# Kernel optimization log

Measured on AMD Instinct MI355X. Metric: run time of the kernel, lower is better.

The kernel has to match this reference:

```python
import jax, jax.numpy as jnp
import numpy as np

B, S, H = 32, 2048, 1024

def setup_inputs() -> dict:
    key = jax.random.key(0)
    k1, k2, k3, k4, k5 = jax.random.split(key, 5)
    return {
        "hidden": jax.random.normal(k1, (B, H), dtype=jnp.float32),
        "encoder_outputs": jax.random.normal(k2, (B, S, H), dtype=jnp.float32),
        "W_attn": jax.random.normal(k3, (H, H), dtype=jnp.float32) * (1.0 / np.sqrt(H)),
        "b_attn": jax.random.normal(k4, (H,), dtype=jnp.float32) * 0.01,
        "v": jax.random.uniform(k5, (H,), dtype=jnp.float32),
    }

def reference(hidden, encoder_outputs, W_attn, b_attn, v):
    # energy = tanh((enc + hidden[:,None,:]) @ W^T + b)  -> [B,S,H]
    x = encoder_outputs + hidden[:, None, :]
    energy = jnp.tanh(jnp.einsum('bsh,oh->bso', x, W_attn) + b_attn)
    scores = jnp.einsum('bsh,h->bs', energy, v)            # [B,S]
    attn_weights = jax.nn.softmax(scores, axis=1)          # [B,S]
    context = jnp.einsum('bs,bsh->bh', attn_weights, encoder_outputs)  # [B,H]
    return (context, attn_weights)
```

## Files before the change

### kernel.cpp

```cpp
#include <hip/hip_runtime.h>
#include <hip/hip_bf16.h>

#define BATCH 32
#define SEQ   2048
#define HID   1024
#define M_TOT (BATCH*SEQ)
#define NG    32

typedef __attribute__((ext_vector_type(8))) short          bf16x8;
typedef __attribute__((ext_vector_type(8))) unsigned short us8;
typedef __attribute__((ext_vector_type(4))) float          f32x4;

__device__ __forceinline__ unsigned short f2bf_rn(float x) {
    unsigned u = __float_as_uint(x);
    return (unsigned short)((u + 0x7fffu + ((u >> 16) & 1u)) >> 16);
}
__device__ __forceinline__ float bf2f(unsigned short h) {
    return __uint_as_float(((unsigned)h) << 16);
}
__device__ __forceinline__ unsigned cvt_pk_bf16(float s0, float s1) {
    unsigned r;
    asm("v_cvt_pk_bf16_f32 %0, %1, %2" : "=v"(r) : "v"(s0), "v"(s1));
    return r;
}

using as1_cv = const __attribute__((address_space(1))) void;
using as3_v  = __attribute__((address_space(3))) void;
__device__ __forceinline__ void gload16(const void* g, char* s) {
    __builtin_amdgcn_global_load_lds((as1_cv*)g, (as3_v*)s, 16, 0, 0);
}

#define FENCE() asm volatile("" ::: "memory")
#define BAR_P()  do { FENCE(); __builtin_amdgcn_s_barrier(); FENCE(); } while (0)
#define BAR_LG() do { asm volatile("s_waitcnt lgkmcnt(0)" ::: "memory"); \
                      __builtin_amdgcn_s_barrier(); FENCE(); } while (0)
#define BAR_VM8() do { asm volatile("s_waitcnt vmcnt(8) lgkmcnt(0)" ::: "memory"); \
                       __builtin_amdgcn_s_barrier(); FENCE(); } while (0)

#define MFMA_BLK(A4, B4, IB) do { \
  _Pragma("unroll") for (int i_ = 0; i_ < 4; i_++) \
  _Pragma("unroll") for (int j_ = 0; j_ < 4; j_++) \
    acc[(IB) + i_][j_] = __builtin_amdgcn_mfma_f32_16x16x32_bf16(A4[i_], B4[j_], acc[(IB)+i_][j_], 0, 0, 0); \
} while (0)

__global__ __launch_bounds__(256) void k_convW(const float* __restrict__ W,
                                               unsigned short* __restrict__ w2) {
    const int i8 = (blockIdx.x * 256 + threadIdx.x) * 8;
    const int o = i8 >> 10, h = i8 & 1023;
    float4 w0 = *(const float4*)(W + i8);
    float4 w1 = *(const float4*)(W + i8 + 4);
    float xs[8] = {w0.x, w0.y, w0.z, w0.w, w1.x, w1.y, w1.z, w1.w};
    us8 hv{}, lv{};
#pragma unroll
    for (int t = 0; t < 8; t++) {
        unsigned short xh = f2bf_rn(xs[t]);
        hv[t] = (unsigned short)xh;
        lv[t] = (unsigned short)f2bf_rn(xs[t] - bf2f(xh));
    }
    *(us8*)(w2 + (size_t)o * 2048 + h)        = hv;
    *(us8*)(w2 + (size_t)o * 2048 + 1024 + h) = lv;
}

__global__ __launch_bounds__(512, 2) void k_gemm_scores(
    const float* __restrict__ enc,
    const float* __restrict__ hidden,
    const unsigned short* __restrict__ w2,
    const float* __restrict__ b_attn,
    const float* __restrict__ v,
    float* __restrict__ pscore16)
{
    extern __shared__ char smem[];
    float* hidL = (float*)(smem + 131072);

    const int tid  = threadIdx.x;
    const int lane = tid & 63, wid = tid >> 6;
    const int wr = wid >> 2, wc = wid & 3;
    const int fr = lane & 15, g = lane >> 4;
    const int gxr = (fr >> 1) & 3;
    const int gsw = (g ^ gxr) * 16;

    const int bid  = blockIdx.x;
    const int swz  = (bid & 7) * 128 + (bid >> 3);
    const int mbase = (swz >> 2) * 256;
    const int nbase = (swz & 3) * 256;
    const int bidx  = mbase >> 11;

    const int arow = tid >> 1;
    const int acol = (tid & 1) * 16;
    const int axr  = (arow >> 1) & 3;
    const int ao0  = (((tid & 1) * 2) ^ axr) * 16;
    const int ao1  = ao0 ^ 16;
    const float* encP = enc + (size_t)(mbase + arow) * HID + acol;

    const int brow  = wid * 16 + (lane >> 2);
    const int bsx8  = ((lane & 3) ^ ((lane >> 3) & 3)) * 8;

    *(float2*)(hidL + tid * 2) = *(const float2*)(hidden + (size_t)bidx * HID + tid * 2);

    f32x4 acc[8][4];
#pragma unroll
    for (int i = 0; i < 8; i++)
#pragma unroll
        for (int j = 0; j < 4; j++) acc[i][j] = (f32x4)0.f;

    float4 er[4];

    auto loadEnc = [&](int Gn) {
        const float* ep = encP + Gn * 32;
#pragma unroll
        for (int q = 0; q < 4; q++) er[q] = *(const float4*)(ep + q * 4);
    };
    auto convA = [&](int Gn) {
        char* ap = smem + (Gn & 1) * 32768 + arow * 64;
        const float* hp = hidL + Gn * 32 + acol;
        unsigned hpk[8], lpk[8];
#pragma unroll
        for (int q = 0; q < 4; q++) {
            float4 e = er[q];
            float4 h = *(const float4*)(hp + q * 4);
            float x0 = e.x + h.x, x1 = e.y + h.y;
            float x2 = e.z + h.z, x3 = e.w + h.w;
            unsigned p01 = cvt_pk_bf16(x0, x1);
            unsigned p23 = cvt_pk_bf16(x2, x3);
            float h0 = __uint_as_float(p01 << 16);
            float h1 = __uint_as_float(p01 & 0xffff0000u);
            float h2 = __uint_as_float(p23 << 16);
            float h3 = __uint_as_float(p23 & 0xffff0000u);
            hpk[q * 2]     = p01;
            hpk[q * 2 + 1] = p23;
            lpk[q * 2]     = cvt_pk_bf16(x0 - h0, x1 - h1);
            lpk[q * 2 + 1] = cvt_pk_bf16(x2 - h2, x3 - h3);
        }
        *(uint4*)(ap + ao0)          = make_uint4(hpk[0], hpk[1], hpk[2], hpk[3]);
        *(uint4*)(ap + ao1)          = make_uint4(hpk[4], hpk[5], hpk[6], hpk[7]);
        *(uint4*)(ap + 16384 + ao0)  = make_uint4(lpk[0], lpk[1], lpk[2], lpk[3]);
        *(uint4*)(ap + 16384 + ao1)  = make_uint4(lpk[4], lpk[5], lpk[6], lpk[7]);
    };
    auto stageB = [&](int G2, int part) {
        const unsigned short* s0 = w2 + (size_t)(nbase + brow) * 2048 + part * 1024 + G2 * 32 + bsx8;
        char* d0 = smem + 65536 + (G2 & 1) * 32768 + part * 16384 + wid * 1024;
        gload16(s0, d0);
        gload16(s0 + (size_t)128 * 2048, d0 + 8192);
    };
    auto rdA = [&](int slot, int part, int i) -> bf16x8 {
        return *(const bf16x8*)(smem + slot * 32768 + part * 16384 +
                                (wr * 128 + i * 16 + fr) * 64 + gsw);
    };
    auto rdB = [&](int slot, int part, int j) -> bf16x8 {
        return *(const bf16x8*)(smem + 65536 + slot * 32768 + part * 16384 +
                                (wc * 64 + j * 16 + fr) * 64 + gsw);
    };

    loadEnc(0);
    stageB(0, 0); stageB(0, 1);
    stageB(1, 0); stageB(1, 1);
    asm volatile("s_waitcnt lgkmcnt(0)" ::: "memory");
    __builtin_amdgcn_s_barrier(); FENCE();
    convA(0);
    loadEnc(1);

    bf16x8 aa[4], aa2[4], bh[4], bl[4];

    for (int G = 0; G < NG; ++G) {
        const int slot = G & 1;
        const int Gs = (G + 2 < NG) ? G + 2 : G;
        const int Ge = (G + 2 < NG) ? G + 2 : NG - 1;
        BAR_VM8();
#pragma unroll
        for (int i = 0; i < 4; i++) aa[i] = rdA(slot, 0, i);
#pragma unroll
        for (int j = 0; j < 4; j++) bh[j] = rdB(slot, 0, j);
#pragma unroll
        for (int j = 0; j < 4; j++) bl[j] = rdB(slot, 1, j);
        __builtin_amdgcn_s_setprio(1);
        MFMA_BLK(aa, bh, 0);
        __builtin_amdgcn_s_setprio(0);
        BAR_LG();
        stageB(Gs, 0);
        __builtin_amdgcn_s_setprio(1);
        MFMA_BLK(aa, bl, 0);
        __builtin_amdgcn_s_setprio(0);
        BAR_P();
#pragma unroll
        for (int i = 0; i < 4; i++) aa2[i] = rdA(slot, 0, 4 + i);
        stageB(Gs, 1);
        __builtin_amdgcn_s_setprio(1);
        MFMA_BLK(aa2, bh, 4);
        __builtin_amdgcn_s_setprio(0);
        BAR_P();
        if (G + 1 < NG) convA(G + 1);
        loadEnc(Ge);
        __builtin_amdgcn_s_setprio(1);
        MFMA_BLK(aa2, bl, 4);
        __builtin_amdgcn_s_setprio(0);
        BAR_P();
#pragma unroll
        for (int i = 0; i < 4; i++) aa[i] = rdA(slot, 1, i);
        __builtin_amdgcn_s_setprio(1);
        MFMA_BLK(aa, bh, 0);
        __builtin_amdgcn_s_setprio(0);
#pragma unroll
        for (int i = 0; i < 4; i++) aa2[i] = rdA(slot, 1, 4 + i);
        __builtin_amdgcn_s_setprio(1);
        MFMA_BLK(aa2, bh, 4);
        __builtin_amdgcn_s_setprio(0);
    }

    float rs[8][4];
#pragma unroll
    for (int i = 0; i < 8; i++)
#pragma unroll
        for (int r = 0; r < 4; r++) rs[i][r] = 0.f;

#pragma unroll
    for (int j = 0; j < 4; j++) {
        const int n = nbase + wc * 64 + j * 16 + fr;
        const float ba = b_attn[n];
        const float vv = v[n];
#pragma unroll
        for (int i = 0; i < 8; i++)
#pragma unroll
            for (int r = 0; r < 4; r++) {
                float e  = acc[i][j][r] + ba;
                float ex = __expf(2.f * e);
                rs[i][r] += (1.f - 2.f / (ex + 1.f)) * vv;
            }
    }
#pragma unroll
    for (int off = 1; off < 16; off <<= 1)
#pragma unroll
        for (int i = 0; i < 8; i++)
#pragma unroll
            for (int r = 0; r < 4; r++) rs[i][r] += __shfl_xor(rs[i][r], off, 64);

    float v0 = 0.f, v1 = 0.f;
#pragma unroll
    for (int i = 0; i < 4; i++)
#pragma unroll
        for (int r = 0; r < 4; r++)
            if (fr == i * 4 + r) { v0 = rs[i][r]; v1 = rs[i + 4][r]; }

    const int plane = (swz & 3) * 4 + wc;
    const size_t pb = (size_t)plane * M_TOT + mbase + wr * 128 + g * 4 + (fr & 3);
    pscore16[pb + (fr >> 2) * 16]      = v0;
    pscore16[pb + (fr >> 2) * 16 + 64] = v1;
}

__global__ __launch_bounds__(256) void k_softmax(const float* __restrict__ ps,
                                                 float* __restrict__ out) {
    const int b = blockIdx.x, t = threadIdx.x;
    __shared__ float red[8];
    float loc[8];
    float lmax = -1e30f;
#pragma unroll
    for (int i = 0; i < 8; i++) {
        const int s = t + i * 256;
        float sc = 0.f;
#pragma unroll
        for (int p = 0; p < 16; p++) sc += ps[(size_t)p * M_TOT + (size_t)b * SEQ + s];
        loc[i] = sc;
        lmax = fmaxf(lmax, sc);
    }
    for (int o = 32; o; o >>= 1) lmax = fmaxf(lmax, __shfl_xor(lmax, o, 64));
    if ((t & 63) == 0) red[t >> 6] = lmax;
    __syncthreads();
    const float bmax = fmaxf(fmaxf(red[0], red[1]), fmaxf(red[2], red[3]));
    float ev[8], lsum = 0.f;
#pragma unroll
    for (int i = 0; i < 8; i++) { ev[i] = expf(loc[i] - bmax); lsum += ev[i]; }
    for (int o = 32; o; o >>= 1) lsum += __shfl_xor(lsum, o, 64);
    __syncthreads();
    if ((t & 63) == 0) red[4 + (t >> 6)] = lsum;
    __syncthreads();
    const float inv = 1.f / (red[4] + red[5] + red[6] + red[7]);
#pragma unroll
    for (int i = 0; i < 8; i++)
        out[(size_t)BATCH * HID + (size_t)b * SEQ + t + i * 256] = ev[i] * inv;
}

__global__ __launch_bounds__(256) void k_pctx(const float* __restrict__ enc,
                                              const float* __restrict__ attn,
                                              float* __restrict__ pctx) {
    const int hc = blockIdx.x, scb = blockIdx.y, b = blockIdx.z;
    const int h = hc * 256 + threadIdx.x;
    const float* ap = attn + (size_t)b * SEQ + scb * 256;
    const float* ep = enc + ((size_t)b * SEQ + scb * 256) * HID + h;
    float a = 0.f;
#pragma unroll 4
    for (int s = 0; s < 256; s++) a += ap[s] * ep[(size_t)s * HID];
    pctx[((size_t)scb * BATCH + b) * HID + h] = a;
}

__global__ __launch_bounds__(256) void k_ctx(const float* __restrict__ pctx,
                                             float* __restrict__ out) {
    const int i = blockIdx.x * 256 + threadIdx.x;
    float a = 0.f;
#pragma unroll
    for (int p = 0; p < 8; p++) a += pctx[(size_t)p * BATCH * HID + i];
    out[i] = a;
}

extern "C" void kernel_launch(void* const* d_in, const int* in_sizes, int n_in,
                              void* d_out, int out_size, void* d_ws, size_t ws_size,
                              hipStream_t stream) {
    const float* hidden = (const float*)d_in[0];
    const float* enc    = (const float*)d_in[1];
    const float* W      = (const float*)d_in[2];
    const float* b_attn = (const float*)d_in[3];
    const float* v      = (const float*)d_in[4];
    float* out = (float*)d_out;

    char* ws = (char*)d_ws;
    unsigned short* w2 = (unsigned short*)ws;
    float* pscore16    = (float*)(ws + ((size_t)4 << 20));
    float* pctx        = (float*)ws;

    const int smemBytes = 131072 + 4096;
    hipFuncSetAttribute((const void*)k_gemm_scores,
                        hipFuncAttributeMaxDynamicSharedMemorySize, smemBytes);

    k_convW<<<dim3(512), dim3(256), 0, stream>>>(W, w2);
    k_gemm_scores<<<dim3(1024), dim3(512), smemBytes, stream>>>(
        enc, hidden, w2, b_attn, v, pscore16);
    k_softmax<<<dim3(BATCH), dim3(256), 0, stream>>>(pscore16, out);
    k_pctx<<<dim3(4, 8, BATCH), dim3(256), 0, stream>>>(enc, out + BATCH * HID, pctx);
    k_ctx<<<dim3(128), dim3(256), 0, stream>>>(pctx, out);
}
```

Before: 405.1 us.

## Triple-buffer B tiles, single-buffer A, cut per-iteration barriers to two

Reworks the GEMM main loop's shared-memory plan. The weight (B) tiles now use three rotating LDS slots, and the converted activation (A) tile uses one slot. Total LDS stays the same. Both B stages for iteration G+2 are issued right after the first fragment reads, and the MFMA blocks are regrouped with sched_barriers so each iteration needs only two workgroup barriers instead of five. The aim is less barrier stall and more overlap of global-to-LDS loads with MFMA work. In exchange, the A conversion for the next step is serialized after all MFMAs finish, and an unused convA stub lambda is left in the code.

```diff
diff --git a/kernel.cpp b/kernel.cpp
--- a/kernel.cpp
+++ b/kernel.cpp
@@ -31,11 +31,7 @@
 }
 
 #define FENCE() asm volatile("" ::: "memory")
-#define BAR_P()  do { FENCE(); __builtin_amdgcn_s_barrier(); FENCE(); } while (0)
-#define BAR_LG() do { asm volatile("s_waitcnt lgkmcnt(0)" ::: "memory"); \
-                      __builtin_amdgcn_s_barrier(); FENCE(); } while (0)
-#define BAR_VM8() do { asm volatile("s_waitcnt vmcnt(8) lgkmcnt(0)" ::: "memory"); \
-                       __builtin_amdgcn_s_barrier(); FENCE(); } while (0)
+#define SCHEDB() __builtin_amdgcn_sched_barrier(0)
 
 #define MFMA_BLK(A4, B4, IB) do { \
   _Pragma("unroll") for (int i_ = 0; i_ < 4; i_++) \
@@ -110,8 +106,13 @@
 #pragma unroll
         for (int q = 0; q < 4; q++) er[q] = *(const float4*)(ep + q * 4);
     };
-    auto convA = [&](int Gn) {
-        char* ap = smem + (Gn & 1) * 32768 + arow * 64;
+    auto convA = [&]() {
+        char* ap = smem + arow * 64;
+        const float* hp = hidL + acol;
+        return ap; (void)hp;
+    };
+    auto doConvA = [&](int Gn) {
+        char* ap = smem + arow * 64;
         const float* hp = hidL + Gn * 32 + acol;
         unsigned hpk[8], lpk[8];
 #pragma unroll
@@ -136,75 +137,75 @@
         *(uint4*)(ap + 16384 + ao0)  = make_uint4(lpk[0], lpk[1], lpk[2], lpk[3]);
         *(uint4*)(ap + 16384 + ao1)  = make_uint4(lpk[4], lpk[5], lpk[6], lpk[7]);
     };
-    auto stageB = [&](int G2, int part) {
+    auto stageB = [&](int G2, int slotW, int part) {
         const unsigned short* s0 = w2 + (size_t)(nbase + brow) * 2048 + part * 1024 + G2 * 32 + bsx8;
-        char* d0 = smem + 65536 + (G2 & 1) * 32768 + part * 16384 + wid * 1024;
+        char* d0 = smem + 32768 + slotW * 32768 + part * 16384 + wid * 1024;
         gload16(s0, d0);
         gload16(s0 + (size_t)128 * 2048, d0 + 8192);
     };
-    auto rdA = [&](int slot, int part, int i) -> bf16x8 {
-        return *(const bf16x8*)(smem + slot * 32768 + part * 16384 +
+    auto rdA = [&](int part, int i) -> bf16x8 {
+        return *(const bf16x8*)(smem + part * 16384 +
                                 (wr * 128 + i * 16 + fr) * 64 + gsw);
     };
-    auto rdB = [&](int slot, int part, int j) -> bf16x8 {
-        return *(const bf16x8*)(smem + 65536 + slot * 32768 + part * 16384 +
+    auto rdB = [&](int slotR, int part, int j) -> bf16x8 {
+        return *(const bf16x8*)(smem + 32768 + slotR * 32768 + part * 16384 +
                                 (wc * 64 + j * 16 + fr) * 64 + gsw);
     };
 
     loadEnc(0);
-    stageB(0, 0); stageB(0, 1);
-    stageB(1, 0); stageB(1, 1);
+    stageB(0, 0, 0); stageB(0, 0, 1);
+    stageB(1, 1, 0); stageB(1, 1, 1);
     asm volatile("s_waitcnt lgkmcnt(0)" ::: "memory");
     __builtin_amdgcn_s_barrier(); FENCE();
-    convA(0);
+    doConvA(0);
     loadEnc(1);
 
     bf16x8 aa[4], aa2[4], bh[4], bl[4];
+    int slotR = 0, slotW = 2;
 
     for (int G = 0; G < NG; ++G) {
-        const int slot = G & 1;
-        const int Gs = (G + 2 < NG) ? G + 2 : G;
-        const int Ge = (G + 2 < NG) ? G + 2 : NG - 1;
-        BAR_VM8();
-#pragma unroll
-        for (int i = 0; i < 4; i++) aa[i] = rdA(slot, 0, i);
-#pragma unroll
-        for (int j = 0; j < 4; j++) bh[j] = rdB(slot, 0, j);
-#pragma unroll
-        for (int j = 0; j < 4; j++) bl[j] = rdB(slot, 1, j);
+        const int G2 = (G + 2 < NG) ? G + 2 : NG - 1;
+        asm volatile("s_waitcnt vmcnt(8) lgkmcnt(0)" ::: "memory");
+        __builtin_amdgcn_s_barrier(); FENCE();
+
+#pragma unroll
+        for (int j = 0; j < 4; j++) bh[j] = rdB(slotR, 0, j);
+#pragma unroll
+        for (int i = 0; i < 4; i++) aa[i] = rdA(0, i);
+        stageB(G2, slotW, 0);
+        stageB(G2, slotW, 1);
+#pragma unroll
+        for (int j = 0; j < 4; j++) bl[j] = rdB(slotR, 1, j);
+#pragma unroll
+        for (int i = 0; i < 4; i++) aa2[i] = rdA(0, 4 + i);
+        __builtin_amdgcn_s_setprio(1);
+        MFMA_BLK(aa, bh, 0);
+        MFMA_BLK(aa, bl, 0);
+        __builtin_amdgcn_s_setprio(0);
+        SCHEDB();
+#pragma unroll
+        for (int i = 0; i < 4; i++) aa[i] = rdA(1, i);
+        __builtin_amdgcn_s_setprio(1);
+        MFMA_BLK(aa2, bh, 4);
+        MFMA_BLK(aa2, bl, 4);
+        __builtin_amdgcn_s_setprio(0);
+        SCHEDB();
+#pragma unroll
+        for (int i = 0; i < 4; i++) aa2[i] = rdA(1, 4 + i);
         __builtin_amdgcn_s_setprio(1);
         MFMA_BLK(aa, bh, 0);
         __builtin_amdgcn_s_setprio(0);
-        BAR_LG();
-        stageB(Gs, 0);
-        __builtin_amdgcn_s_setprio(1);
-        MFMA_BLK(aa, bl, 0);
-        __builtin_amdgcn_s_setprio(0);
-        BAR_P();
-#pragma unroll
-        for (int i = 0; i < 4; i++) aa2[i] = rdA(slot, 0, 4 + i);
-        stageB(Gs, 1);
         __builtin_amdgcn_s_setprio(1);
         MFMA_BLK(aa2, bh, 4);
         __builtin_amdgcn_s_setprio(0);
-        BAR_P();
-        if (G + 1 < NG) convA(G + 1);
-        loadEnc(Ge);
-        __builtin_amdgcn_s_setprio(1);
-        MFMA_BLK(aa2, bl, 4);
-        __builtin_amdgcn_s_setprio(0);
-        BAR_P();
-#pragma unroll
-        for (int i = 0; i < 4; i++) aa[i] = rdA(slot, 1, i);
-        __builtin_amdgcn_s_setprio(1);
-        MFMA_BLK(aa, bh, 0);
-        __builtin_amdgcn_s_setprio(0);
-#pragma unroll
-        for (int i = 0; i < 4; i++) aa2[i] = rdA(slot, 1, 4 + i);
-        __builtin_amdgcn_s_setprio(1);
-        MFMA_BLK(aa2, bh, 4);
-        __builtin_amdgcn_s_setprio(0);
+
+        FENCE(); __builtin_amdgcn_s_barrier(); FENCE();
+        if (G + 1 < NG) doConvA(G + 1);
+        loadEnc(G2);
+        slotR = (slotR == 2) ? 0 : slotR + 1;
+        slotW = (slotW == 2) ? 0 : slotW + 1;
     }
+    (void)convA;
 
     float rs[8][4];
 #pragma unroll
```

Measured after the change: 786.5 us. 1.94x slower.

## Precompute hidden@W^T+b per batch and drop hidden add from GEMM A-conversion

Applied to the files above, without the earlier changes.

Uses linearity to split (enc+hidden)W^T into enc W^T plus a per-batch bias hidden W^T + b, computed by a new small kernel k_hw. The main GEMM no longer stages hidden in LDS or adds it during bf16 split conversion, which frees shared memory and removes per-element adds. It also reworks the pipeline barriers, replacing the vmcnt-based wait with lgkm barriers, reordering the B-fragment reads, and skipping out-of-range prefetches. This adds an extra launch and a change in rounding, since hidden is no longer folded into the bf16 hi/lo split.

```diff
diff --git a/kernel.cpp b/kernel.cpp
--- a/kernel.cpp
+++ b/kernel.cpp
@@ -34,8 +34,6 @@
 #define BAR_P()  do { FENCE(); __builtin_amdgcn_s_barrier(); FENCE(); } while (0)
 #define BAR_LG() do { asm volatile("s_waitcnt lgkmcnt(0)" ::: "memory"); \
                       __builtin_amdgcn_s_barrier(); FENCE(); } while (0)
-#define BAR_VM8() do { asm volatile("s_waitcnt vmcnt(8) lgkmcnt(0)" ::: "memory"); \
-                       __builtin_amdgcn_s_barrier(); FENCE(); } while (0)
 
 #define MFMA_BLK(A4, B4, IB) do { \
   _Pragma("unroll") for (int i_ = 0; i_ < 4; i_++) \
@@ -61,16 +59,35 @@
     *(us8*)(w2 + (size_t)o * 2048 + 1024 + h) = lv;
 }
 
+__global__ __launch_bounds__(256) void k_hw(const float* __restrict__ W,
+                                            const float* __restrict__ hidden,
+                                            const float* __restrict__ b_attn,
+                                            float* __restrict__ cb) {
+    __shared__ float hid[HID];
+    const int t = threadIdx.x, b = blockIdx.y;
+#pragma unroll
+    for (int i = 0; i < 4; i++)
+        hid[t + i * 256] = hidden[(size_t)b * HID + t + i * 256];
+    __syncthreads();
+    const int n = blockIdx.x * 256 + t;
+    const float* wr = W + (size_t)n * HID;
+    float a = 0.f;
+#pragma unroll 4
+    for (int k = 0; k < HID; k += 4) {
+        float4 w4 = *(const float4*)(wr + k);
+        a += w4.x * hid[k] + w4.y * hid[k + 1] + w4.z * hid[k + 2] + w4.w * hid[k + 3];
+    }
+    cb[(size_t)b * HID + n] = a + b_attn[n];
+}
+
 __global__ __launch_bounds__(512, 2) void k_gemm_scores(
     const float* __restrict__ enc,
-    const float* __restrict__ hidden,
     const unsigned short* __restrict__ w2,
-    const float* __restrict__ b_attn,
+    const float* __restrict__ cb,
     const float* __restrict__ v,
     float* __restrict__ pscore16)
 {
     extern __shared__ char smem[];
-    float* hidL = (float*)(smem + 131072);
 
     const int tid  = threadIdx.x;
     const int lane = tid & 63, wid = tid >> 6;
@@ -95,8 +112,6 @@
     const int brow  = wid * 16 + (lane >> 2);
     const int bsx8  = ((lane & 3) ^ ((lane >> 3) & 3)) * 8;
 
-    *(float2*)(hidL + tid * 2) = *(const float2*)(hidden + (size_t)bidx * HID + tid * 2);
-
     f32x4 acc[8][4];
 #pragma unroll
     for (int i = 0; i < 8; i++)
@@ -112,24 +127,20 @@
     };
     auto convA = [&](int Gn) {
         char* ap = smem + (Gn & 1) * 32768 + arow * 64;
-        const float* hp = hidL + Gn * 32 + acol;
         unsigned hpk[8], lpk[8];
 #pragma unroll
         for (int q = 0; q < 4; q++) {
             float4 e = er[q];
-            float4 h = *(const float4*)(hp + q * 4);
-            float x0 = e.x + h.x, x1 = e.y + h.y;
-            float x2 = e.z + h.z, x3 = e.w + h.w;
-            unsigned p01 = cvt_pk_bf16(x0, x1);
-            unsigned p23 = cvt_pk_bf16(x2, x3);
+            unsigned p01 = cvt_pk_bf16(e.x, e.y);
+            unsigned p23 = cvt_pk_bf16(e.z, e.w);
             float h0 = __uint_as_float(p01 << 16);
             float h1 = __uint_as_float(p01 & 0xffff0000u);
             float h2 = __uint_as_float(p23 << 16);
             float h3 = __uint_as_float(p23 & 0xffff0000u);
             hpk[q * 2]     = p01;
             hpk[q * 2 + 1] = p23;
-            lpk[q * 2]     = cvt_pk_bf16(x0 - h0, x1 - h1);
-            lpk[q * 2 + 1] = cvt_pk_bf16(x2 - h2, x3 - h3);
+            lpk[q * 2]     = cvt_pk_bf16(e.x - h0, e.y - h1);
+            lpk[q * 2 + 1] = cvt_pk_bf16(e.z - h2, e.w - h3);
         }
         *(uint4*)(ap + ao0)          = make_uint4(hpk[0], hpk[1], hpk[2], hpk[3]);
         *(uint4*)(ap + ao1)          = make_uint4(hpk[4], hpk[5], hpk[6], hpk[7]);
@@ -151,11 +162,10 @@
                                 (wc * 64 + j * 16 + fr) * 64 + gsw);
     };
 
+    stageB(0, 0); stageB(0, 1);
+    FENCE();
     loadEnc(0);
-    stageB(0, 0); stageB(0, 1);
     stageB(1, 0); stageB(1, 1);
-    asm volatile("s_waitcnt lgkmcnt(0)" ::: "memory");
-    __builtin_amdgcn_s_barrier(); FENCE();
     convA(0);
     loadEnc(1);
 
@@ -163,33 +173,31 @@
 
     for (int G = 0; G < NG; ++G) {
         const int slot = G & 1;
-        const int Gs = (G + 2 < NG) ? G + 2 : G;
-        const int Ge = (G + 2 < NG) ? G + 2 : NG - 1;
-        BAR_VM8();
+        BAR_LG();
 #pragma unroll
         for (int i = 0; i < 4; i++) aa[i] = rdA(slot, 0, i);
 #pragma unroll
         for (int j = 0; j < 4; j++) bh[j] = rdB(slot, 0, j);
+        __builtin_amdgcn_s_setprio(1);
+        MFMA_BLK(aa, bh, 0);
+        __builtin_amdgcn_s_setprio(0);
+        BAR_LG();
 #pragma unroll
         for (int j = 0; j < 4; j++) bl[j] = rdB(slot, 1, j);
-        __builtin_amdgcn_s_setprio(1);
-        MFMA_BLK(aa, bh, 0);
+        if (G + 2 < NG) stageB(G + 2, 0);
+        __builtin_amdgcn_s_setprio(1);
+        MFMA_BLK(aa, bl, 0);
         __builtin_amdgcn_s_setprio(0);
         BAR_LG();
-        stageB(Gs, 0);
-        __builtin_amdgcn_s_setprio(1);
-        MFMA_BLK(aa, bl, 0);
-        __builtin_amdgcn_s_setprio(0);
-        BAR_P();
 #pragma unroll
         for (int i = 0; i < 4; i++) aa2[i] = rdA(slot, 0, 4 + i);
-        stageB(Gs, 1);
+        if (G + 2 < NG) stageB(G + 2, 1);
         __builtin_amdgcn_s_setprio(1);
         MFMA_BLK(aa2, bh, 4);
         __builtin_amdgcn_s_setprio(0);
         BAR_P();
         if (G + 1 < NG) convA(G + 1);
-        loadEnc(Ge);
+        if (G + 2 < NG) loadEnc(G + 2);
         __builtin_amdgcn_s_setprio(1);
         MFMA_BLK(aa2, bl, 4);
         __builtin_amdgcn_s_setprio(0);
@@ -215,7 +223,7 @@
 #pragma unroll
     for (int j = 0; j < 4; j++) {
         const int n = nbase + wc * 64 + j * 16 + fr;
-        const float ba = b_attn[n];
+        const float ba = cb[(size_t)bidx * HID + n];
         const float vv = v[n];
 #pragma unroll
         for (int i = 0; i < 8; i++)
@@ -313,15 +321,17 @@
     char* ws = (char*)d_ws;
     unsigned short* w2 = (unsigned short*)ws;
     float* pscore16    = (float*)(ws + ((size_t)4 << 20));
+    float* cb          = (float*)(ws + ((size_t)8 << 20));
     float* pctx        = (float*)ws;
 
-    const int smemBytes = 131072 + 4096;
+    const int smemBytes = 131072;
     hipFuncSetAttribute((const void*)k_gemm_scores,
                         hipFuncAttributeMaxDynamicSharedMemorySize, smemBytes);
 
     k_convW<<<dim3(512), dim3(256), 0, stream>>>(W, w2);
+    k_hw<<<dim3(4, 32), dim3(256), 0, stream>>>(W, hidden, b_attn, cb);
     k_gemm_scores<<<dim3(1024), dim3(512), smemBytes, stream>>>(
-        enc, hidden, w2, b_attn, v, pscore16);
+        enc, w2, cb, v, pscore16);
     k_softmax<<<dim3(BATCH), dim3(256), 0, stream>>>(pscore16, out);
     k_pctx<<<dim3(4, 8, BATCH), dim3(256), 0, stream>>>(enc, out + BATCH * HID, pctx);
     k_ctx<<<dim3(128), dim3(256), 0, stream>>>(pctx, out);
```

Result: slower. 455.9 us (+12.5%).
